# Performance work log

Hardware: AMD Instinct MI355X
Metric: run time of the kernel (lower is better)

The kernel has to match this reference:

```python
import jax, jax.numpy as jnp
import numpy as np

TOP_K = 2


def setup_inputs() -> dict:
    key = jax.random.key(0)
    ks = jax.random.split(key, 6)
    B, S, H, I, E = 4, 2048, 1024, 4096, 8
    x = jax.random.normal(ks[0], (B, S, H), dtype=jnp.float32)
    Wr = jax.random.normal(ks[1], (H, E), dtype=jnp.float32) * (1.0 / np.sqrt(H))
    W1 = jax.random.normal(ks[2], (E, H, I), dtype=jnp.float32) * (1.0 / np.sqrt(H))
    b1 = jnp.zeros((E, I), dtype=jnp.float32)
    W2 = jax.random.normal(ks[3], (E, I, H), dtype=jnp.float32) * (1.0 / np.sqrt(I))
    b2 = jnp.zeros((E, H), dtype=jnp.float32)
    return {"x": x, "Wr": Wr, "W1": W1, "b1": b1, "W2": W2, "b2": b2}


def reference(x, Wr, W1, b1, W2, b2):
    B, S, H = x.shape
    E = Wr.shape[1]
    xf = x.reshape(-1, H)                              # [T, H], T = B*S
    logits = xf @ Wr                                   # [T, E]
    probs = jax.nn.softmax(logits, axis=-1)
    rw, sel = jax.lax.top_k(probs, TOP_K)              # [T, K]
    rw = rw / jnp.sum(rw, axis=-1, keepdims=True)
    out = jnp.zeros_like(xf)
    # Loop over small fixed expert count; each token contributes only via its
    # top-k combine weight (zero weight == not routed, matching index_add).
    for i in range(E):
        wi = jnp.sum(jnp.where(sel == i, rw, 0.0), axis=-1)    # [T]
        h = jax.nn.silu(xf @ W1[i] + b1[i])                    # [T, I]
        out = out + (h @ W2[i] + b2[i]) * wi[:, None]
    return out.reshape(B, S, H)
```

## Files before the change

kernel.cpp:

```cpp
#include <hip/hip_runtime.h>
#include <cstdint>
#include <cstddef>

#define TTOK 8192
#define HDIM 1024
#define IDIM 4096
#define NEXP 8
#define PMAX 18432
#define WS_NEED 302260352ULL

#define STG 24576

typedef __attribute__((ext_vector_type(8))) short bf16x8;
typedef __attribute__((ext_vector_type(4))) float f32x4;

#define AS3 __attribute__((address_space(3)))
#define AS1 __attribute__((address_space(1)))

__device__ __forceinline__ void gld16(const void* g, void* s) {
  __builtin_amdgcn_global_load_lds((const AS1 void*)g, (AS3 void*)s, 16, 0, 0);
}

__device__ __forceinline__ unsigned short f2b(float f) {
  unsigned u = __builtin_bit_cast(unsigned, f);
  unsigned r = ((u >> 16) & 1u) + 0x7FFFu;
  return (unsigned short)((u + r) >> 16);
}

__global__ __launch_bounds__(256, 2) void router_k(
    const float* __restrict__ x, const float* __restrict__ wr,
    unsigned short* __restrict__ xb, int* __restrict__ t2e,
    float* __restrict__ t2w)
{
  const int t = blockIdx.x * 4 + (threadIdx.x >> 6);
  const int l = threadIdx.x & 63;
  const float* xr = x + (size_t)t * HDIM;
  float acc[8] = {0.f,0.f,0.f,0.f,0.f,0.f,0.f,0.f};
  #pragma unroll
  for (int j = 0; j < 4; ++j) {
    const int base = j * 256 + l * 4;
    const float4 xv = *(const float4*)(xr + base);
    const float xa[4] = {xv.x, xv.y, xv.z, xv.w};
    ushort4 ub;
    ub.x = f2b(xa[0]); ub.y = f2b(xa[1]); ub.z = f2b(xa[2]); ub.w = f2b(xa[3]);
    *(ushort4*)(xb + (size_t)t * HDIM + base) = ub;
    #pragma unroll
    for (int ii = 0; ii < 4; ++ii) {
      const float4 w0 = *(const float4*)(wr + (size_t)(base + ii) * 8);
      const float4 w1 = *(const float4*)(wr + (size_t)(base + ii) * 8 + 4);
      acc[0] += xa[ii] * w0.x; acc[1] += xa[ii] * w0.y;
      acc[2] += xa[ii] * w0.z; acc[3] += xa[ii] * w0.w;
      acc[4] += xa[ii] * w1.x; acc[5] += xa[ii] * w1.y;
      acc[6] += xa[ii] * w1.z; acc[7] += xa[ii] * w1.w;
    }
  }
  #pragma unroll
  for (int e = 0; e < 8; ++e) {
    float v = acc[e];
    #pragma unroll
    for (int off = 32; off > 0; off >>= 1) v += __shfl_xor(v, off);
    acc[e] = v;
  }
  if (l == 0) {
    float l0 = -1e30f; int i0 = 0;
    #pragma unroll
    for (int e = 0; e < 8; ++e) if (acc[e] > l0) { l0 = acc[e]; i0 = e; }
    float l1 = -1e30f; int i1 = (i0 == 0) ? 1 : 0;
    #pragma unroll
    for (int e = 0; e < 8; ++e) if (e != i0 && acc[e] > l1) { l1 = acc[e]; i1 = e; }
    const float w0 = 1.f / (1.f + expf(l1 - l0));
    t2e[t * 2] = i0; t2e[t * 2 + 1] = i1;
    t2w[t * 2] = w0; t2w[t * 2 + 1] = 1.f - w0;
  }
}

__global__ void count_k(const int* __restrict__ t2e, int* __restrict__ meta) {
  const int t = threadIdx.x, w = t >> 6, l = t & 63;
  int cnt[8] = {0,0,0,0,0,0,0,0};
  for (int c = 0; c < 16; ++c) {
    const int tok = (w * 16 + c) * 64 + l;
    const int e0 = t2e[2 * tok], e1 = t2e[2 * tok + 1];
    #pragma unroll
    for (int e = 0; e < 8; ++e)
      cnt[e] += __popcll(__ballot(e0 == e)) + __popcll(__ballot(e1 == e));
  }
  __shared__ int part[8][8];
  if (l == 0) {
    #pragma unroll
    for (int e = 0; e < 8; ++e) part[w][e] = cnt[e];
  }
  __syncthreads();
  if (t == 0) {
    int off = 0;
    #pragma unroll
    for (int e = 0; e < 8; ++e) {
      int s = 0;
      #pragma unroll
      for (int w2 = 0; w2 < 8; ++w2) s += part[w2][e];
      meta[e] = s; meta[16 + e] = off; off += (s + 255) & ~255;
    }
    meta[24] = off;
  }
}

__global__ void scatter_k(const int* __restrict__ t2e, const int* __restrict__ meta,
                          int* __restrict__ ltok, int* __restrict__ t2p)
{
  const int e = blockIdx.x;
  const int t = threadIdx.x, w = t >> 6, l = t & 63;
  const int off = meta[16 + e];
  const int cnt = meta[e];
  __shared__ int wsum[4];
  __shared__ int base;
  if (t == 0) base = 0;
  __syncthreads();
  const unsigned long long lt = (1ULL << l) - 1ULL;
  for (int c = 0; c < TTOK / 256; ++c) {
    const int tok = c * 256 + t;
    const bool m0 = (t2e[2 * tok] == e);
    const bool m1 = (t2e[2 * tok + 1] == e);
    const unsigned long long b0 = __ballot(m0);
    const unsigned long long b1 = __ballot(m1);
    const int n0 = __popcll(b0), n1 = __popcll(b1);
    const int r0 = __popcll(b0 & lt);
    const int r1 = n0 + __popcll(b1 & lt);
    if (l == 0) wsum[w] = n0 + n1;
    __syncthreads();
    int wb = base;
    #pragma unroll
    for (int i = 0; i < 4; ++i) if (i < w) wb += wsum[i];
    const int tot = wsum[0] + wsum[1] + wsum[2] + wsum[3];
    __syncthreads();
    if (t == 0) base += tot;
    if (m0) { const int p = off + wb + r0; ltok[p] = tok; t2p[2 * tok] = p; }
    if (m1) { const int p = off + wb + r1; ltok[p] = tok; t2p[2 * tok + 1] = p; }
    __syncthreads();
  }
  const int padded = (cnt + 255) & ~255;
  for (int i = cnt + t; i < padded; i += 256) ltok[off + i] = -1;
}

__global__ __launch_bounds__(256, 2) void packT_k(const float* __restrict__ src,
                                                  unsigned short* __restrict__ dst,
                                                  int K, int N)
{
  const int tiles_n = N >> 8, tiles_k = K >> 5;
  const int bid = blockIdx.x;
  const int e = bid / (tiles_k * tiles_n);
  const int rem = bid % (tiles_k * tiles_n);
  const int kt = rem / tiles_n, it = rem % tiles_n;
  const float* S = src + (size_t)e * K * N + (size_t)kt * 32 * N + (size_t)it * 256;
  unsigned short* D = dst + (size_t)e * N * K + (size_t)it * 256 * K + (size_t)kt * 32;
  __shared__ uint32_t lds[256 * 17];
  const int t = threadIdx.x;
  #pragma unroll
  for (int q = 0; q < 4; ++q) {
    const int task = q * 256 + t;
    const int i4 = task & 63, kp = task >> 6;
    const float* p0 = S + (size_t)(2 * kp) * N + i4 * 4;
    const float4 r0 = *(const float4*)p0;
    const float4 r1 = *(const float4*)(p0 + N);
    const float a0[4] = {r0.x, r0.y, r0.z, r0.w};
    const float a1[4] = {r1.x, r1.y, r1.z, r1.w};
    #pragma unroll
    for (int j = 0; j < 4; ++j)
      lds[(i4 * 4 + j) * 17 + kp] = (uint32_t)f2b(a0[j]) | ((uint32_t)f2b(a1[j]) << 16);
  }
  __syncthreads();
  #pragma unroll
  for (int r = 0; r < 4; ++r) {
    const int idx = r * 256 + t;
    const int il = idx >> 2, q4 = idx & 3;
    uint4 o;
    o.x = lds[il * 17 + q4 * 4 + 0];
    o.y = lds[il * 17 + q4 * 4 + 1];
    o.z = lds[il * 17 + q4 * 4 + 2];
    o.w = lds[il * 17 + q4 * 4 + 3];
    *(uint4*)(D + (size_t)il * K + q4 * 8) = o;
  }
}


__global__ __launch_bounds__(512, 4) void gemm1_k(
    const unsigned short* __restrict__ xb, const unsigned short* __restrict__ w1t,
    const float* __restrict__ b1, const int* __restrict__ meta,
    const int* __restrict__ ltok, unsigned short* __restrict__ h)
{
  const int wg = blockIdx.x;
  const int id = (wg & 7) * (2304 / 8) + (wg >> 3);
  const int mt = id >> 5, nt = id & 31;
  if (mt * 256 >= meta[24]) return;
  int e = 0;
  #pragma unroll
  for (int i = 1; i < 8; ++i) if (meta[16 + i] <= mt * 256) e = i;

  extern __shared__ char lds[];
  const int t = threadIdx.x;
  const int w = t >> 6, l = t & 63;
  const int wn = w & 1, wm = w >> 1;

  const unsigned short* asrc;
  {
    const int G = t;
    const int line = G >> 3, q = (G & 7) ^ (line & 7);
    const int row = 2 * line + (q >> 2), g = q & 3;
    asrc = w1t + ((size_t)e * IDIM + nt * 128 + row) * HDIM + g * 8;
  }
  const unsigned short* bsrc[2];
  #pragma unroll
  for (int c = 0; c < 2; ++c) {
    const int G = c * 512 + t;
    const int line = G >> 3, q = (G & 7) ^ (line & 7);
    const int row = 2 * line + (q >> 2), g = q & 3;
    int tok = ltok[mt * 256 + row]; if (tok < 0) tok = 0;
    bsrc[c] = xb + (size_t)tok * HDIM + g * 8;
  }

  const int lr = l & 15, lg = l >> 4;
  const int p_r = (((lr & 1) << 2) + lg) ^ (lr >> 1);
  const int aoff = (wn * 32 + (lr >> 1)) * 128 + p_r * 16;
  const int boff = 8192 + (wm * 32 + (lr >> 1)) * 128 + p_r * 16;

  f32x4 acc[4][4] = {};

  auto STAGE = [&](int tile) {
    const int ks = tile * 32;
    char* sb = lds + (tile % 3) * STG;
    gld16(asrc + ks, sb + w * 1024);
    gld16(bsrc[0] + ks, sb + 8192 + w * 1024);
    gld16(bsrc[1] + ks, sb + 16384 + w * 1024);
  };

  STAGE(0); STAGE(1);
  const int NT = HDIM / 32;
  for (int kt = 0; kt < NT; ++kt) {
    if (kt + 2 < NT) {
      STAGE(kt + 2);
      asm volatile("s_waitcnt vmcnt(6)" ::: "memory");
    } else if (kt + 1 < NT) {
      asm volatile("s_waitcnt vmcnt(3)" ::: "memory");
    } else {
      asm volatile("s_waitcnt vmcnt(0)" ::: "memory");
    }
    __builtin_amdgcn_s_barrier();
    const char* ab = lds + (kt % 3) * STG;
    bf16x8 af[4], bf[4];
    #pragma unroll
    for (int fm = 0; fm < 4; ++fm) af[fm] = *(const bf16x8*)(ab + aoff + fm * 1024);
    #pragma unroll
    for (int fn = 0; fn < 4; ++fn) bf[fn] = *(const bf16x8*)(ab + boff + fn * 1024);
    __builtin_amdgcn_s_setprio(1);
    #pragma unroll
    for (int fm = 0; fm < 4; ++fm)
      #pragma unroll
      for (int fn = 0; fn < 4; ++fn)
        acc[fm][fn] = __builtin_amdgcn_mfma_f32_16x16x32_bf16(af[fm], bf[fn], acc[fm][fn], 0, 0, 0);
    __builtin_amdgcn_s_setprio(0);
    __builtin_amdgcn_s_barrier();
  }

  const int lg4 = lg * 4;
  #pragma unroll
  for (int fm = 0; fm < 4; ++fm) {
    const int ib = nt * 128 + wn * 64 + fm * 16 + lg4;
    const float4 b1v = *(const float4*)(b1 + e * IDIM + ib);
    #pragma unroll
    for (int fn = 0; fn < 4; ++fn) {
      const int trow = mt * 256 + wm * 64 + fn * 16 + lr;
      const float v0 = acc[fm][fn][0] + b1v.x;
      const float v1 = acc[fm][fn][1] + b1v.y;
      const float v2 = acc[fm][fn][2] + b1v.z;
      const float v3 = acc[fm][fn][3] + b1v.w;
      ushort4 st;
      st.x = f2b(v0 / (1.f + __expf(-v0)));
      st.y = f2b(v1 / (1.f + __expf(-v1)));
      st.z = f2b(v2 / (1.f + __expf(-v2)));
      st.w = f2b(v3 / (1.f + __expf(-v3)));
      *(ushort4*)(h + (size_t)trow * IDIM + ib) = st;
    }
  }
}

__global__ __launch_bounds__(512, 4) void gemm2_k(
    const unsigned short* __restrict__ h, const unsigned short* __restrict__ w2t,
    const int* __restrict__ meta, float* __restrict__ y)
{
  const int wg = blockIdx.x;
  const int id = (wg & 7) * (576 / 8) + (wg >> 3);
  const int mt = id >> 3, nt = id & 7;
  if (mt * 256 >= meta[24]) return;
  int e = 0;
  #pragma unroll
  for (int i = 1; i < 8; ++i) if (meta[16 + i] <= mt * 256) e = i;

  extern __shared__ char lds[];
  const int t = threadIdx.x;
  const int w = t >> 6, l = t & 63;
  const int wn = w & 1, wm = w >> 1;

  const unsigned short* asrc;
  {
    const int G = t;
    const int line = G >> 3, q = (G & 7) ^ (line & 7);
    const int row = 2 * line + (q >> 2), g = q & 3;
    asrc = w2t + ((size_t)e * HDIM + nt * 128 + row) * IDIM + g * 8;
  }
  const unsigned short* bsrc[2];
  #pragma unroll
  for (int c = 0; c < 2; ++c) {
    const int G = c * 512 + t;
    const int line = G >> 3, q = (G & 7) ^ (line & 7);
    const int row = 2 * line + (q >> 2), g = q & 3;
    bsrc[c] = h + (size_t)(mt * 256 + row) * IDIM + g * 8;
  }

  const int lr = l & 15, lg = l >> 4;
  const int p_r = (((lr & 1) << 2) + lg) ^ (lr >> 1);
  const int aoff = (wn * 32 + (lr >> 1)) * 128 + p_r * 16;
  const int boff = 8192 + (wm * 32 + (lr >> 1)) * 128 + p_r * 16;

  f32x4 acc[4][4] = {};

  auto STAGE = [&](int tile) {
    const int ks = tile * 32;
    char* sb = lds + (tile % 3) * STG;
    gld16(asrc + ks, sb + w * 1024);
    gld16(bsrc[0] + ks, sb + 8192 + w * 1024);
    gld16(bsrc[1] + ks, sb + 16384 + w * 1024);
  };

  STAGE(0); STAGE(1);
  const int NT = IDIM / 32;
  for (int kt = 0; kt < NT; ++kt) {
    if (kt + 2 < NT) {
      STAGE(kt + 2);
      asm volatile("s_waitcnt vmcnt(6)" ::: "memory");
    } else if (kt + 1 < NT) {
      asm volatile("s_waitcnt vmcnt(3)" ::: "memory");
    } else {
      asm volatile("s_waitcnt vmcnt(0)" ::: "memory");
    }
    __builtin_amdgcn_s_barrier();
    const char* ab = lds + (kt % 3) * STG;
    bf16x8 af[4], bf[4];
    #pragma unroll
    for (int fm = 0; fm < 4; ++fm) af[fm] = *(const bf16x8*)(ab + aoff + fm * 1024);
    #pragma unroll
    for (int fn = 0; fn < 4; ++fn) bf[fn] = *(const bf16x8*)(ab + boff + fn * 1024);
    __builtin_amdgcn_s_setprio(1);
    #pragma unroll
    for (int fm = 0; fm < 4; ++fm)
      #pragma unroll
      for (int fn = 0; fn < 4; ++fn)
        acc[fm][fn] = __builtin_amdgcn_mfma_f32_16x16x32_bf16(af[fm], bf[fn], acc[fm][fn], 0, 0, 0);
    __builtin_amdgcn_s_setprio(0);
    __builtin_amdgcn_s_barrier();
  }

  const int lg4 = lg * 4;
  #pragma unroll
  for (int fm = 0; fm < 4; ++fm) {
    const int colb = nt * 128 + wn * 64 + fm * 16 + lg4;
    #pragma unroll
    for (int fn = 0; fn < 4; ++fn) {
      const int row = mt * 256 + wm * 64 + fn * 16 + lr;
      float4 st;
      st.x = acc[fm][fn][0]; st.y = acc[fm][fn][1];
      st.z = acc[fm][fn][2]; st.w = acc[fm][fn][3];
      *(float4*)(y + (size_t)row * HDIM + colb) = st;
    }
  }
}

__global__ __launch_bounds__(256, 4) void combine_k(
    const float* __restrict__ y, const float* __restrict__ b2,
    const int* __restrict__ t2e, const float* __restrict__ t2w,
    const int* __restrict__ t2p, float* __restrict__ out)
{
  const int t = blockIdx.x * 4 + (threadIdx.x >> 6);
  const int l = threadIdx.x & 63;
  const int e0 = t2e[t * 2], e1 = t2e[t * 2 + 1];
  const float w0 = t2w[t * 2], w1v = t2w[t * 2 + 1];
  const int p0 = t2p[t * 2], p1 = t2p[t * 2 + 1];
  const float* y0 = y + (size_t)p0 * HDIM;
  const float* y1 = y + (size_t)p1 * HDIM;
  const float* bb0 = b2 + e0 * HDIM;
  const float* bb1 = b2 + e1 * HDIM;
  float* o = out + (size_t)t * HDIM;
  #pragma unroll
  for (int j = 0; j < 4; ++j) {
    const int c = j * 256 + l * 4;
    const float4 a = *(const float4*)(y0 + c);
    const float4 b = *(const float4*)(y1 + c);
    const float4 c0 = *(const float4*)(bb0 + c);
    const float4 c1 = *(const float4*)(bb1 + c);
    float4 r;
    r.x = w0 * (a.x + c0.x) + w1v * (b.x + c1.x);
    r.y = w0 * (a.y + c0.y) + w1v * (b.y + c1.y);
    r.z = w0 * (a.z + c0.z) + w1v * (b.z + c1.z);
    r.w = w0 * (a.w + c0.w) + w1v * (b.w + c1.w);
    *(float4*)(o + c) = r;
  }
}

__global__ void sentinel_k(float* out) { out[0] = 1.0e6f; }

extern "C" void kernel_launch(void* const* d_in, const int* in_sizes, int n_in,
                              void* d_out, int out_size, void* d_ws, size_t ws_size,
                              hipStream_t stream)
{
  (void)in_sizes; (void)n_in; (void)out_size;
  const float* x  = (const float*)d_in[0];
  const float* wr = (const float*)d_in[1];
  const float* w1 = (const float*)d_in[2];
  const float* b1 = (const float*)d_in[3];
  const float* w2 = (const float*)d_in[4];
  const float* b2 = (const float*)d_in[5];
  float* out = (float*)d_out;
  char* ws = (char*)d_ws;

  if (ws_size < WS_NEED) { sentinel_k<<<1, 1, 0, stream>>>(out); return; }

  unsigned short* xb  = (unsigned short*)(ws);
  unsigned short* w1t = (unsigned short*)(ws + 16777216);
  unsigned short* w2t = (unsigned short*)(ws + 83886080);
  unsigned short* h   = (unsigned short*)(ws + 150994944);
  int*   t2e  = (int*)(ws + 301989888);
  float* t2w  = (float*)(ws + 302055424);
  int*   ltok = (int*)(ws + 302120960);
  int*   t2p  = (int*)(ws + 302194688);
  int*   meta = (int*)(ws + 302260224);
  float* y    = (float*)(ws);

  hipFuncSetAttribute((const void*)gemm1_k, hipFuncAttributeMaxDynamicSharedMemorySize, 3 * STG);
  hipFuncSetAttribute((const void*)gemm2_k, hipFuncAttributeMaxDynamicSharedMemorySize, 3 * STG);

  router_k<<<TTOK / 4, 256, 0, stream>>>(x, wr, xb, t2e, t2w);
  packT_k<<<NEXP * (HDIM / 32) * (IDIM / 256), 256, 0, stream>>>(w1, w1t, HDIM, IDIM);
  packT_k<<<NEXP * (IDIM / 32) * (HDIM / 256), 256, 0, stream>>>(w2, w2t, IDIM, HDIM);
  count_k<<<1, 512, 0, stream>>>(t2e, meta);
  scatter_k<<<NEXP, 256, 0, stream>>>(t2e, meta, ltok, t2p);

  gemm1_k<<<72 * 32, 512, 3 * STG, stream>>>(xb, w1t, b1, meta, ltok, h);
  gemm2_k<<<72 * 8, 512, 3 * STG, stream>>>(h, w2t, meta, y);
  combine_k<<<TTOK / 4, 256, 0, stream>>>(y, b2, t2e, t2w, t2p, out);
}
```

Measured before the change: 550.4 us.

## Shrink expert GEMM tiles to 128x128 with 4 waves and reorder prefetch

Both expert GEMMs move from 256x128 tiles with 512 threads to 128x128 tiles with 256 threads, doubling the grid and cutting LDS per block from 72KB to 48KB. Each wave still computes a 64x64 subtile. The next-stage global-to-LDS prefetch is now issued after the current fragments are read from LDS, and sched_barrier fences pin the barriers in place. This aims at more resident blocks, less padding waste at expert boundaries and better load balance, at the cost of reloading each weight tile for twice as many token tiles.

```diff
diff --git a/kernel.cpp b/kernel.cpp
--- a/kernel.cpp
+++ b/kernel.cpp
@@ -9,7 +9,7 @@
 #define PMAX 18432
 #define WS_NEED 302260352ULL
 
-#define STG 24576
+#define SLOT 16384
 
 typedef __attribute__((ext_vector_type(8))) short bf16x8;
 typedef __attribute__((ext_vector_type(4))) float f32x4;
@@ -19,6 +19,12 @@
 
 __device__ __forceinline__ void gld16(const void* g, void* s) {
   __builtin_amdgcn_global_load_lds((const AS1 void*)g, (AS3 void*)s, 16, 0, 0);
+}
+
+__device__ __forceinline__ void pinned_barrier() {
+  __builtin_amdgcn_sched_barrier(0);
+  __builtin_amdgcn_s_barrier();
+  __builtin_amdgcn_sched_barrier(0);
 }
 
 __device__ __forceinline__ unsigned short f2b(float f) {
@@ -181,74 +187,70 @@
 }
 
 
-__global__ __launch_bounds__(512, 4) void gemm1_k(
+__global__ __launch_bounds__(256, 3) void gemm1_k(
     const unsigned short* __restrict__ xb, const unsigned short* __restrict__ w1t,
     const float* __restrict__ b1, const int* __restrict__ meta,
     const int* __restrict__ ltok, unsigned short* __restrict__ h)
 {
   const int wg = blockIdx.x;
-  const int id = (wg & 7) * (2304 / 8) + (wg >> 3);
+  const int id = (wg & 7) * (4608 / 8) + (wg >> 3);
   const int mt = id >> 5, nt = id & 31;
-  if (mt * 256 >= meta[24]) return;
+  if (mt * 128 >= meta[24]) return;
   int e = 0;
   #pragma unroll
-  for (int i = 1; i < 8; ++i) if (meta[16 + i] <= mt * 256) e = i;
+  for (int i = 1; i < 8; ++i) if (meta[16 + i] <= mt * 128) e = i;
 
   extern __shared__ char lds[];
   const int t = threadIdx.x;
   const int w = t >> 6, l = t & 63;
   const int wn = w & 1, wm = w >> 1;
 
-  const unsigned short* asrc;
-  {
-    const int G = t;
+  const unsigned short* asrc[2]; const unsigned short* bsrc[2];
+  #pragma unroll
+  for (int c = 0; c < 2; ++c) {
+    const int G = c * 256 + t;
     const int line = G >> 3, q = (G & 7) ^ (line & 7);
     const int row = 2 * line + (q >> 2), g = q & 3;
-    asrc = w1t + ((size_t)e * IDIM + nt * 128 + row) * HDIM + g * 8;
-  }
-  const unsigned short* bsrc[2];
-  #pragma unroll
-  for (int c = 0; c < 2; ++c) {
-    const int G = c * 512 + t;
-    const int line = G >> 3, q = (G & 7) ^ (line & 7);
-    const int row = 2 * line + (q >> 2), g = q & 3;
-    int tok = ltok[mt * 256 + row]; if (tok < 0) tok = 0;
+    asrc[c] = w1t + ((size_t)e * IDIM + nt * 128 + row) * HDIM + g * 8;
+    int tok = ltok[mt * 128 + row]; if (tok < 0) tok = 0;
     bsrc[c] = xb + (size_t)tok * HDIM + g * 8;
   }
 
   const int lr = l & 15, lg = l >> 4;
-  const int p_r = (((lr & 1) << 2) + lg) ^ (lr >> 1);
-  const int aoff = (wn * 32 + (lr >> 1)) * 128 + p_r * 16;
-  const int boff = 8192 + (wm * 32 + (lr >> 1)) * 128 + p_r * 16;
-
   f32x4 acc[4][4] = {};
 
-  auto STAGE = [&](int tile) {
-    const int ks = tile * 32;
-    char* sb = lds + (tile % 3) * STG;
-    gld16(asrc + ks, sb + w * 1024);
+  auto STAGE = [&](int kt) {
+    char* sb = lds + (kt % 3) * SLOT;
+    const int ks = kt * 32;
+    gld16(asrc[0] + ks, sb + w * 1024);
+    gld16(asrc[1] + ks, sb + 4096 + w * 1024);
     gld16(bsrc[0] + ks, sb + 8192 + w * 1024);
-    gld16(bsrc[1] + ks, sb + 16384 + w * 1024);
+    gld16(bsrc[1] + ks, sb + 12288 + w * 1024);
   };
 
   STAGE(0); STAGE(1);
   const int NT = HDIM / 32;
   for (int kt = 0; kt < NT; ++kt) {
-    if (kt + 2 < NT) {
-      STAGE(kt + 2);
-      asm volatile("s_waitcnt vmcnt(6)" ::: "memory");
-    } else if (kt + 1 < NT) {
-      asm volatile("s_waitcnt vmcnt(3)" ::: "memory");
+    if (kt + 1 < NT) {
+      asm volatile("s_waitcnt vmcnt(4)" ::: "memory");
     } else {
       asm volatile("s_waitcnt vmcnt(0)" ::: "memory");
     }
-    __builtin_amdgcn_s_barrier();
-    const char* ab = lds + (kt % 3) * STG;
+    pinned_barrier();
+    const char* sl = lds + (kt % 3) * SLOT;
     bf16x8 af[4], bf[4];
     #pragma unroll
-    for (int fm = 0; fm < 4; ++fm) af[fm] = *(const bf16x8*)(ab + aoff + fm * 1024);
-    #pragma unroll
-    for (int fn = 0; fn < 4; ++fn) bf[fn] = *(const bf16x8*)(ab + boff + fn * 1024);
+    for (int f = 0; f < 4; ++f) {
+      const int rowA = wn * 64 + f * 16 + lr;
+      const int lineA = rowA >> 1;
+      const int pA = (((rowA & 1) << 2) + lg) ^ (lineA & 7);
+      af[f] = *(const bf16x8*)(sl + lineA * 128 + pA * 16);
+      const int rowB = wm * 64 + f * 16 + lr;
+      const int lineB = rowB >> 1;
+      const int pB = (((rowB & 1) << 2) + lg) ^ (lineB & 7);
+      bf[f] = *(const bf16x8*)(sl + 8192 + lineB * 128 + pB * 16);
+    }
+    if (kt + 2 < NT) STAGE(kt + 2);
     __builtin_amdgcn_s_setprio(1);
     #pragma unroll
     for (int fm = 0; fm < 4; ++fm)
@@ -256,7 +258,7 @@
       for (int fn = 0; fn < 4; ++fn)
         acc[fm][fn] = __builtin_amdgcn_mfma_f32_16x16x32_bf16(af[fm], bf[fn], acc[fm][fn], 0, 0, 0);
     __builtin_amdgcn_s_setprio(0);
-    __builtin_amdgcn_s_barrier();
+    pinned_barrier();
   }
 
   const int lg4 = lg * 4;
@@ -266,7 +268,7 @@
     const float4 b1v = *(const float4*)(b1 + e * IDIM + ib);
     #pragma unroll
     for (int fn = 0; fn < 4; ++fn) {
-      const int trow = mt * 256 + wm * 64 + fn * 16 + lr;
+      const int trow = mt * 128 + wm * 64 + fn * 16 + lr;
       const float v0 = acc[fm][fn][0] + b1v.x;
       const float v1 = acc[fm][fn][1] + b1v.y;
       const float v2 = acc[fm][fn][2] + b1v.z;
@@ -281,72 +283,68 @@
   }
 }
 
-__global__ __launch_bounds__(512, 4) void gemm2_k(
+__global__ __launch_bounds__(256, 3) void gemm2_k(
     const unsigned short* __restrict__ h, const unsigned short* __restrict__ w2t,
     const int* __restrict__ meta, float* __restrict__ y)
 {
   const int wg = blockIdx.x;
-  const int id = (wg & 7) * (576 / 8) + (wg >> 3);
+  const int id = (wg & 7) * (1152 / 8) + (wg >> 3);
   const int mt = id >> 3, nt = id & 7;
-  if (mt * 256 >= meta[24]) return;
+  if (mt * 128 >= meta[24]) return;
   int e = 0;
   #pragma unroll
-  for (int i = 1; i < 8; ++i) if (meta[16 + i] <= mt * 256) e = i;
+  for (int i = 1; i < 8; ++i) if (meta[16 + i] <= mt * 128) e = i;
 
   extern __shared__ char lds[];
   const int t = threadIdx.x;
   const int w = t >> 6, l = t & 63;
   const int wn = w & 1, wm = w >> 1;
 
-  const unsigned short* asrc;
-  {
-    const int G = t;
+  const unsigned short* asrc[2]; const unsigned short* bsrc[2];
+  #pragma unroll
+  for (int c = 0; c < 2; ++c) {
+    const int G = c * 256 + t;
     const int line = G >> 3, q = (G & 7) ^ (line & 7);
     const int row = 2 * line + (q >> 2), g = q & 3;
-    asrc = w2t + ((size_t)e * HDIM + nt * 128 + row) * IDIM + g * 8;
-  }
-  const unsigned short* bsrc[2];
-  #pragma unroll
-  for (int c = 0; c < 2; ++c) {
-    const int G = c * 512 + t;
-    const int line = G >> 3, q = (G & 7) ^ (line & 7);
-    const int row = 2 * line + (q >> 2), g = q & 3;
-    bsrc[c] = h + (size_t)(mt * 256 + row) * IDIM + g * 8;
+    asrc[c] = w2t + ((size_t)e * HDIM + nt * 128 + row) * IDIM + g * 8;
+    bsrc[c] = h + (size_t)(mt * 128 + row) * IDIM + g * 8;
   }
 
   const int lr = l & 15, lg = l >> 4;
-  const int p_r = (((lr & 1) << 2) + lg) ^ (lr >> 1);
-  const int aoff = (wn * 32 + (lr >> 1)) * 128 + p_r * 16;
-  const int boff = 8192 + (wm * 32 + (lr >> 1)) * 128 + p_r * 16;
-
   f32x4 acc[4][4] = {};
 
-  auto STAGE = [&](int tile) {
-    const int ks = tile * 32;
-    char* sb = lds + (tile % 3) * STG;
-    gld16(asrc + ks, sb + w * 1024);
+  auto STAGE = [&](int kt) {
+    char* sb = lds + (kt % 3) * SLOT;
+    const int ks = kt * 32;
+    gld16(asrc[0] + ks, sb + w * 1024);
+    gld16(asrc[1] + ks, sb + 4096 + w * 1024);
     gld16(bsrc[0] + ks, sb + 8192 + w * 1024);
-    gld16(bsrc[1] + ks, sb + 16384 + w * 1024);
+    gld16(bsrc[1] + ks, sb + 12288 + w * 1024);
   };
 
   STAGE(0); STAGE(1);
   const int NT = IDIM / 32;
   for (int kt = 0; kt < NT; ++kt) {
-    if (kt + 2 < NT) {
-      STAGE(kt + 2);
-      asm volatile("s_waitcnt vmcnt(6)" ::: "memory");
-    } else if (kt + 1 < NT) {
-      asm volatile("s_waitcnt vmcnt(3)" ::: "memory");
+    if (kt + 1 < NT) {
+      asm volatile("s_waitcnt vmcnt(4)" ::: "memory");
     } else {
       asm volatile("s_waitcnt vmcnt(0)" ::: "memory");
     }
-    __builtin_amdgcn_s_barrier();
-    const char* ab = lds + (kt % 3) * STG;
+    pinned_barrier();
+    const char* sl = lds + (kt % 3) * SLOT;
     bf16x8 af[4], bf[4];
     #pragma unroll
-    for (int fm = 0; fm < 4; ++fm) af[fm] = *(const bf16x8*)(ab + aoff + fm * 1024);
-    #pragma unroll
-    for (int fn = 0; fn < 4; ++fn) bf[fn] = *(const bf16x8*)(ab + boff + fn * 1024);
+    for (int f = 0; f < 4; ++f) {
+      const int rowA = wn * 64 + f * 16 + lr;
+      const int lineA = rowA >> 1;
+      const int pA = (((rowA & 1) << 2) + lg) ^ (lineA & 7);
+      af[f] = *(const bf16x8*)(sl + lineA * 128 + pA * 16);
+      const int rowB = wm * 64 + f * 16 + lr;
+      const int lineB = rowB >> 1;
+      const int pB = (((rowB & 1) << 2) + lg) ^ (lineB & 7);
+      bf[f] = *(const bf16x8*)(sl + 8192 + lineB * 128 + pB * 16);
+    }
+    if (kt + 2 < NT) STAGE(kt + 2);
     __builtin_amdgcn_s_setprio(1);
     #pragma unroll
     for (int fm = 0; fm < 4; ++fm)
@@ -354,7 +352,7 @@
       for (int fn = 0; fn < 4; ++fn)
         acc[fm][fn] = __builtin_amdgcn_mfma_f32_16x16x32_bf16(af[fm], bf[fn], acc[fm][fn], 0, 0, 0);
     __builtin_amdgcn_s_setprio(0);
-    __builtin_amdgcn_s_barrier();
+    pinned_barrier();
   }
 
   const int lg4 = lg * 4;
@@ -363,7 +361,7 @@
     const int colb = nt * 128 + wn * 64 + fm * 16 + lg4;
     #pragma unroll
     for (int fn = 0; fn < 4; ++fn) {
-      const int row = mt * 256 + wm * 64 + fn * 16 + lr;
+      const int row = mt * 128 + wm * 64 + fn * 16 + lr;
       float4 st;
       st.x = acc[fm][fn][0]; st.y = acc[fm][fn][1];
       st.z = acc[fm][fn][2]; st.w = acc[fm][fn][3];
@@ -432,8 +430,8 @@
   int*   meta = (int*)(ws + 302260224);
   float* y    = (float*)(ws);
 
-  hipFuncSetAttribute((const void*)gemm1_k, hipFuncAttributeMaxDynamicSharedMemorySize, 3 * STG);
-  hipFuncSetAttribute((const void*)gemm2_k, hipFuncAttributeMaxDynamicSharedMemorySize, 3 * STG);
+  hipFuncSetAttribute((const void*)gemm1_k, hipFuncAttributeMaxDynamicSharedMemorySize, 3 * SLOT);
+  hipFuncSetAttribute((const void*)gemm2_k, hipFuncAttributeMaxDynamicSharedMemorySize, 3 * SLOT);
 
   router_k<<<TTOK / 4, 256, 0, stream>>>(x, wr, xb, t2e, t2w);
   packT_k<<<NEXP * (HDIM / 32) * (IDIM / 256), 256, 0, stream>>>(w1, w1t, HDIM, IDIM);
@@ -441,7 +439,7 @@
   count_k<<<1, 512, 0, stream>>>(t2e, meta);
   scatter_k<<<NEXP, 256, 0, stream>>>(t2e, meta, ltok, t2p);
 
-  gemm1_k<<<72 * 32, 512, 3 * STG, stream>>>(xb, w1t, b1, meta, ltok, h);
-  gemm2_k<<<72 * 8, 512, 3 * STG, stream>>>(h, w2t, meta, y);
+  gemm1_k<<<144 * 32, 256, 3 * SLOT, stream>>>(xb, w1t, b1, meta, ltok, h);
+  gemm2_k<<<144 * 8, 256, 3 * SLOT, stream>>>(h, w2t, meta, y);
   combine_k<<<TTOK / 4, 256, 0, stream>>>(y, b2, t2e, t2w, t2p, out);
 }
```

After: 583.9 us. 1.06x slower.
